# Performance work log

Hardware: AMD Instinct MI355X
Metric: run time of the kernel (lower is better)

The kernel has to match this reference:

```python
import jax, jax.numpy as jnp
import numpy as np

B, T, D, H = 4, 1024, 512, 8
DK = D // H
P = 2 * T - 1  # relative position length


def rel_shift(x):
    # x: (b, h, t, 2t-1) -> (b, h, t, t), Transformer-XL relative shift
    b, h, t, p = x.shape
    x = jnp.pad(x, ((0, 0), (0, 0), (0, 0), (1, 0)))  # (b,h,t,p+1)
    x = x.reshape(b, h, p + 1, t)[:, :, 1:, :].reshape(b, h, t, p)
    return x[..., :t]


def setup_inputs() -> dict:
    key = jax.random.key(0)
    ks = jax.random.split(key, 16)
    s = 0.02
    return {
        "q": jax.random.normal(ks[0], (B, T, D), jnp.float32),
        "k": jax.random.normal(ks[1], (B, T, D), jnp.float32),
        "v": jax.random.normal(ks[2], (B, T, D), jnp.float32),
        "pos_emb": jax.random.normal(ks[3], (1, P, D), jnp.float32),
        "Wq": jax.random.normal(ks[4], (D, D), jnp.float32) * s,
        "bq": jnp.zeros((D,), jnp.float32),
        "Wk": jax.random.normal(ks[5], (D, D), jnp.float32) * s,
        "bk": jnp.zeros((D,), jnp.float32),
        "Wv": jax.random.normal(ks[6], (D, D), jnp.float32) * s,
        "bv": jnp.zeros((D,), jnp.float32),
        "Wp": jax.random.normal(ks[7], (D, D), jnp.float32) * s,
        "pos_bias_u": jax.random.normal(ks[8], (H, DK), jnp.float32) * s,
        "pos_bias_v": jax.random.normal(ks[9], (H, DK), jnp.float32) * s,
        "Wo": jax.random.normal(ks[10], (D, D), jnp.float32) * s,
        "bo": jnp.zeros((D,), jnp.float32),
    }


def reference(q, k, v, pos_emb, Wq, bq, Wk, bk, Wv, bv, Wp,
              pos_bias_u, pos_bias_v, Wo, bo):
    b, t, d = q.shape
    # QKV projections, split heads -> (b, t, h, dk)
    qh = (q @ Wq.T + bq).reshape(b, t, H, DK)
    kh = (k @ Wk.T + bk).reshape(b, t, H, DK)
    vh = (v @ Wv.T + bv).reshape(b, t, H, DK)
    # positional projection (no bias): (1, P, h, dk)
    ph = (pos_emb @ Wp.T).reshape(pos_emb.shape[1], H, DK)
    # content term: (q + u) . k
    q_u = qh + pos_bias_u  # (b,t,h,dk)
    matrix_ac = jnp.einsum("bqhd,bkhd->bhqk", q_u, kh)
    # position term: (q + v) . p, then relative shift
    q_v = qh + pos_bias_v
    matrix_bd = jnp.einsum("bqhd,phd->bhqp", q_v, ph)
    matrix_bd = rel_shift(matrix_bd)  # (b,h,t,t)
    scores = (matrix_ac + matrix_bd) / jnp.sqrt(jnp.float32(DK))
    attn = jax.nn.softmax(scores, axis=-1)
    out = jnp.einsum("bhqk,bkhd->bqhd", attn, vh).reshape(b, t, d)
    return out @ Wo.T + bo
```

## Files before the change

### kernel.cpp

```cpp
#include <hip/hip_runtime.h>
#include <math.h>

typedef unsigned short u16;
typedef _Float16 f16;
typedef __attribute__((ext_vector_type(8))) _Float16 f16x8;
typedef __attribute__((ext_vector_type(4))) float f32x4;

#define B_  4
#define T_  1024
#define D_  512
#define H_  8
#define DK_ 64
#define P_  2047

#define MFMAH(a, b, c) __builtin_amdgcn_mfma_f32_16x16x32_f16(a, b, c, 0, 0, 0)

__device__ __forceinline__ u16 f2hbits(float x) {
    union { f16 h; u16 u; } cv; cv.h = (f16)x; return cv.u;
}

__device__ __forceinline__ void gload_lds16(const u16* g, u16* l) {
    __builtin_amdgcn_global_load_lds(
        (const __attribute__((address_space(1))) void*)g,
        (__attribute__((address_space(3))) void*)l, 16, 0, 0);
}

__device__ __forceinline__ int swz8(int row, int colbase) {
    return row * 64 + (((colbase >> 3) ^ (row & 7)) << 3);
}

__global__ __launch_bounds__(256)
void conv_all(const float* __restrict__ q, const float* __restrict__ k,
              const float* __restrict__ v, const float* __restrict__ pe,
              const float* __restrict__ wq, const float* __restrict__ wk,
              const float* __restrict__ wv, const float* __restrict__ wp,
              const float* __restrict__ wo,
              u16* qs, u16* ks, u16* vs, u16* pes,
              u16* wqs, u16* wks, u16* wvs, u16* wps, u16* wos)
{
    const int NQ = 524288;
    const int NPE = 262016;
    const int NW = 65536;
    const int TOT = 3 * NQ + NPE + 5 * NW;
    for (int i = blockIdx.x * 256 + threadIdx.x; i < TOT; i += gridDim.x * 256) {
        const float* src; u16* dst; int off;
        int j = i;
        if (j < NQ)              { src = q;  dst = qs;  off = j; }
        else if ((j -= NQ) < NQ) { src = k;  dst = ks;  off = j; }
        else if ((j -= NQ) < NQ) { src = v;  dst = vs;  off = j; }
        else if ((j -= NQ) < NPE){ src = pe; dst = pes; off = j; }
        else if ((j -= NPE) < NW){ src = wq; dst = wqs; off = j; }
        else if ((j -= NW) < NW) { src = wk; dst = wks; off = j; }
        else if ((j -= NW) < NW) { src = wv; dst = wvs; off = j; }
        else if ((j -= NW) < NW) { src = wp; dst = wps; off = j; }
        else                     { j -= NW; src = wo; dst = wos; off = j; }
        float4 x = *(const float4*)(src + (size_t)off * 4);
        union { f16 h[4]; uint2 u2; } cv;
        cv.h[0] = (f16)x.x; cv.h[1] = (f16)x.y;
        cv.h[2] = (f16)x.z; cv.h[3] = (f16)x.w;
        *(uint2*)(dst + (size_t)off * 4) = cv.u2;
    }
}

__device__ __forceinline__ void gemm_core(
    const u16* __restrict__ A, const u16* __restrict__ Bw,
    int bm, int bn, int M, f32x4 (&acc)[4][4],
    u16 (&sA)[128][64], u16 (&sB)[128][64])
{
    const int tid = threadIdx.x;
    const int ln = tid & 63, w = tid >> 6;
    const int arow = ln & 15, kseg = ln >> 4;
    const int wr = w >> 1, wc = w & 1;

    for (int k0 = 0; k0 < 512; k0 += 64) {
        #pragma unroll
        for (int it = 0; it < 4; ++it) {
            int ch = it * 256 + tid;
            int r = ch >> 3, j = ch & 7;
            int rm = bm + r; if (rm > M - 1) rm = M - 1;
            gload_lds16(A + (size_t)rm * 512 + k0 + ((j ^ (r & 7)) << 3),
                        &sA[0][0] + ch * 8);
        }
        #pragma unroll
        for (int it = 0; it < 4; ++it) {
            int ch = it * 256 + tid;
            int r = ch >> 3, j = ch & 7;
            gload_lds16(Bw + (size_t)(bn + r) * 512 + k0 + ((j ^ (r & 7)) << 3),
                        &sB[0][0] + ch * 8);
        }
        __syncthreads();

        f16x8 af[4][2], bf[4][2];
        #pragma unroll
        for (int mi = 0; mi < 4; ++mi) {
            int row = wr * 64 + mi * 16 + arow;
            #pragma unroll
            for (int kc = 0; kc < 2; ++kc)
                af[mi][kc] = *(const f16x8*)
                    (&sA[row][0] + ((((kc << 2) | kseg) ^ (row & 7)) << 3));
        }
        #pragma unroll
        for (int nj = 0; nj < 4; ++nj) {
            int row = wc * 64 + nj * 16 + arow;
            #pragma unroll
            for (int kc = 0; kc < 2; ++kc)
                bf[nj][kc] = *(const f16x8*)
                    (&sB[row][0] + ((((kc << 2) | kseg) ^ (row & 7)) << 3));
        }
        #pragma unroll
        for (int mi = 0; mi < 4; ++mi)
            #pragma unroll
            for (int nj = 0; nj < 4; ++nj)
                #pragma unroll
                for (int kc = 0; kc < 2; ++kc)
                    acc[mi][nj] = MFMAH(af[mi][kc], bf[nj][kc], acc[mi][nj]);
        __syncthreads();
    }
}

__global__ __launch_bounds__(256, 3)
void gemm_qkvp(const u16* __restrict__ qs, const u16* __restrict__ ks,
               const u16* __restrict__ vs, const u16* __restrict__ pes,
               const u16* __restrict__ wqs, const u16* __restrict__ wks,
               const u16* __restrict__ wvs, const u16* __restrict__ wps,
               const float* __restrict__ bq, const float* __restrict__ bk,
               const float* __restrict__ bv,
               const float* __restrict__ pbu, const float* __restrict__ pbv,
               u16* __restrict__ qub, u16* __restrict__ qvb,
               u16* __restrict__ kh, u16* __restrict__ vt, u16* __restrict__ ph)
{
    __shared__ u16 sA[128][64];
    __shared__ u16 sB[128][64];

    const int by = blockIdx.y;
    const u16 *A, *Bw; const float* bias;
    int seg, bm, M, Tn;
    if (by < 32)      { seg=0; bm=by*128;       A=qs;  Bw=wqs; bias=bq;      M=4096; Tn=T_; }
    else if (by < 64) { seg=1; bm=(by-32)*128;  A=ks;  Bw=wks; bias=bk;      M=4096; Tn=T_; }
    else if (by < 96) { seg=2; bm=(by-64)*128;  A=vs;  Bw=wvs; bias=bv;      M=4096; Tn=T_; }
    else              { seg=3; bm=(by-96)*128;  A=pes; Bw=wps; bias=nullptr; M=P_;   Tn=P_; }
    const int bn = blockIdx.x * 128;

    f32x4 acc[4][4] = {};
    gemm_core(A, Bw, bm, bn, M, acc, sA, sB);

    const int tid = threadIdx.x;
    const int ln = tid & 63, w = tid >> 6;
    const int arow = ln & 15, kseg = ln >> 4;
    const int wr = w >> 1, wc = w & 1;

    float bv0[4];
    #pragma unroll
    for (int nj = 0; nj < 4; ++nj)
        bv0[nj] = bias ? bias[bn + wc * 64 + nj * 16 + arow] : 0.f;

    #pragma unroll
    for (int mi = 0; mi < 4; ++mi)
        #pragma unroll
        for (int r = 0; r < 4; ++r) {
            int m = bm + wr * 64 + mi * 16 + kseg * 4 + r;
            if (m >= M) continue;
            #pragma unroll
            for (int nj = 0; nj < 4; ++nj) {
                int n = bn + wc * 64 + nj * 16 + arow;
                float val = acc[mi][nj][r] + bv0[nj];
                if (seg == 0) {
                    int bb = m >> 10, t = m & 1023;
                    int hh = n >> 6, d = n & 63;
                    size_t off = ((size_t)(bb * H_ + hh) * T_ + t) * 64 + d;
                    qub[off] = f2hbits((val + pbu[hh * 64 + d]) * 0.125f);
                    qvb[off] = f2hbits((val + pbv[hh * 64 + d]) * 0.125f);
                } else if (seg == 2) {
                    int bb = m >> 10, t = m & 1023;
                    int hh = n >> 6, d = n & 63;
                    vt[((size_t)(bb * H_ + hh) * 64 + d) * T_ + t] = f2hbits(val);
                } else {
                    int bb = (Tn == T_) ? (m >> 10) : 0;
                    int t = m - bb * Tn;
                    int hh = n >> 6, d = n & 63;
                    size_t off = ((size_t)(bb * H_ + hh) * Tn + t) * 64 + d;
                    if (seg == 1) kh[off] = f2hbits(val);
                    else          ph[off] = f2hbits(val);
                }
            }
        }
}

__global__ __launch_bounds__(256, 3)
void gemm_out(const u16* __restrict__ A, const u16* __restrict__ Bw,
              const float* __restrict__ bias, float* __restrict__ C)
{
    __shared__ u16 sA[128][64];
    __shared__ u16 sB[128][64];
    const int bn = blockIdx.x * 128;
    const int bm = blockIdx.y * 128;
    f32x4 acc[4][4] = {};
    gemm_core(A, Bw, bm, bn, 4096, acc, sA, sB);

    const int tid = threadIdx.x;
    const int ln = tid & 63, w = tid >> 6;
    const int arow = ln & 15, kseg = ln >> 4;
    const int wr = w >> 1, wc = w & 1;
    #pragma unroll
    for (int mi = 0; mi < 4; ++mi)
        #pragma unroll
        for (int r = 0; r < 4; ++r) {
            int m = bm + wr * 64 + mi * 16 + kseg * 4 + r;
            #pragma unroll
            for (int nj = 0; nj < 4; ++nj) {
                int n = bn + wc * 64 + nj * 16 + arow;
                C[(size_t)m * 512 + n] = acc[mi][nj][r] + bias[n];
            }
        }
}

__global__ __launch_bounds__(256, 2)
void relattn_mfma(const u16* __restrict__ qub, const u16* __restrict__ qvb,
                  const u16* __restrict__ kh, const u16* __restrict__ vt,
                  const u16* __restrict__ ph,
                  u16* __restrict__ ao)
{
    __shared__ u16 s_k[3][64][64];
    __shared__ u16 s_p[3][64][64];
    __shared__ u16 s_pp[4][16][64];

    const int tid = threadIdx.x;
    const int ln  = tid & 63;
    const int w   = tid >> 6;
    const int arow = ln & 15;
    const int kseg = ln >> 4;

    const int lg = ((blockIdx.x & 7) << 6) | (blockIdx.x >> 3);
    const int qt = lg & 15, h = (lg >> 4) & 7, b = lg >> 7;
    const int q0 = qt * 64;

    const size_t kvbase = (size_t)(b * H_ + h) * T_ * 64;
    const size_t vtbase = (size_t)(b * H_ + h) * 64 * T_;
    const size_t pbase  = (size_t)h * P_ * 64;
    const int jb0 = 960 - q0;

    f16x8 qu[2], qv[2];
    {
        const u16* qb = qub + kvbase + (size_t)(q0 + w * 16 + arow) * 64;
        const u16* vb = qvb + kvbase + (size_t)(q0 + w * 16 + arow) * 64;
        #pragma unroll
        for (int c = 0; c < 2; ++c) {
            qu[c] = *(const f16x8*)(qb + c * 32 + kseg * 8);
            qv[c] = *(const f16x8*)(vb + c * 32 + kseg * 8);
        }
    }

    f32x4 o_[4] = {};
    float l_run[4] = {};

    auto stage_k = [&](int kt, int slot) {
        #pragma unroll
        for (int it = 0; it < 2; ++it) {
            int idx = tid + it * 256;
            int r = idx >> 3, ch = idx & 7;
            const u16* src = kh + kvbase + (size_t)(kt * 64 + r) * 64 + ((ch ^ (r & 7)) << 3);
            gload_lds16(src, &s_k[slot][0][0] + idx * 8);
        }
    };
    auto stage_p = [&](int c, int slot) {
        #pragma unroll
        for (int it = 0; it < 2; ++it) {
            int idx = tid + it * 256;
            int r = idx >> 3, ch = idx & 7;
            int j = jb0 + c * 64 + r; if (j > P_ - 1) j = P_ - 1;
            const u16* src = ph + pbase + (size_t)j * 64 + ((ch ^ (r & 7)) << 3);
            gload_lds16(src, &s_p[slot][0][0] + idx * 8);
        }
    };
    auto bd_chunk = [&](int slot, f32x4* out) {
        #pragma unroll
        for (int nb = 0; nb < 4; ++nb) {
            int pr = nb * 16 + arow;
            f16x8 b0 = *(const f16x8*)(&s_p[slot][0][0] + swz8(pr, kseg * 8));
            f16x8 b1 = *(const f16x8*)(&s_p[slot][0][0] + swz8(pr, 32 + kseg * 8));
            out[nb] = MFMAH(qv[0], b0, out[nb]);
            out[nb] = MFMAH(qv[1], b1, out[nb]);
        }
    };

    stage_k(0, 0); stage_k(1, 1);
    stage_p(0, 0); stage_p(1, 1); stage_p(2, 2);
    __syncthreads();
    f32x4 carry[4] = {};
    bd_chunk(0, carry);
    asm volatile("" ::: "memory");
    __builtin_amdgcn_s_barrier();
    asm volatile("" ::: "memory");

    int ks = 0;
    for (int t = 0; t < 16; ++t) {
        const int k0 = t * 64;
        const int pr = (ks + 1 > 2) ? 0 : ks + 1;
        const int kw = (ks + 2 > 2) ? ks - 1 : ks + 2;

        f16x8 vfr[4][2];
        #pragma unroll
        for (int nt = 0; nt < 4; ++nt) {
            const u16* vp = vt + vtbase + (size_t)(nt * 16 + arow) * T_ + k0 + kseg * 8;
            vfr[nt][0] = *(const f16x8*)vp;
            vfr[nt][1] = *(const f16x8*)(vp + 32);
        }

        if (t < 14) { stage_k(t + 2, kw); stage_p(t + 3, ks); }

        __builtin_amdgcn_s_setprio(1);
        f32x4 ac[4] = {};
        #pragma unroll
        for (int nt = 0; nt < 4; ++nt) {
            int kr = nt * 16 + arow;
            f16x8 b0 = *(const f16x8*)(&s_k[ks][0][0] + swz8(kr, kseg * 8));
            f16x8 b1 = *(const f16x8*)(&s_k[ks][0][0] + swz8(kr, 32 + kseg * 8));
            ac[nt] = MFMAH(qu[0], b0, ac[nt]);
            ac[nt] = MFMAH(qu[1], b1, ac[nt]);
        }
        f32x4 bdn[4] = {};
        bd_chunk(pr, bdn);
        __builtin_amdgcn_s_setprio(0);

        float win[5][4];
        #pragma unroll
        for (int r = 0; r < 4; ++r) {
            if (w == 0)      { win[0][r]=carry[3][r]; win[1][r]=bdn[0][r];   win[2][r]=bdn[1][r];   win[3][r]=bdn[2][r];   win[4][r]=bdn[3][r]; }
            else if (w == 1) { win[0][r]=carry[2][r]; win[1][r]=carry[3][r]; win[2][r]=bdn[0][r];   win[3][r]=bdn[1][r];   win[4][r]=bdn[2][r]; }
            else if (w == 2) { win[0][r]=carry[1][r]; win[1][r]=carry[2][r]; win[2][r]=carry[3][r]; win[3][r]=bdn[0][r];   win[4][r]=bdn[1][r]; }
            else             { win[0][r]=carry[0][r]; win[1][r]=carry[1][r]; win[2][r]=carry[2][r]; win[3][r]=carry[3][r]; win[4][r]=bdn[0][r]; }
        }

        #pragma unroll
        for (int r = 0; r < 4; ++r) {
            int sl  = 15 - (kseg << 2) - r;
            int src = (ln & 48) | ((arow + sl) & 15);
            bool hi = (arow < sl);
            int r16 = kseg * 4 + r;
            #pragma unroll
            for (int nt = 0; nt < 4; ++nt) {
                float sel = hi ? win[nt + 1][r] : win[nt][r];
                float pm = __shfl(sel, src, 64);
                float pv = __expf(ac[nt][r] + pm);
                l_run[r] += pv;
                int kl = nt * 16 + arow;
                s_pp[w][r16][(((kl >> 3) ^ (r16 & 7)) << 3) | (kl & 7)] = f2hbits(pv);
            }
        }
        asm volatile("s_waitcnt lgkmcnt(0)" ::: "memory");
        __builtin_amdgcn_sched_barrier(0);

        f16x8 pa0 = *(const f16x8*)(&s_pp[w][arow][0] + ((kseg ^ (arow & 7)) << 3));
        f16x8 pa1 = *(const f16x8*)(&s_pp[w][arow][0] + (((4 + kseg) ^ (arow & 7)) << 3));
        __builtin_amdgcn_s_setprio(1);
        #pragma unroll
        for (int nt = 0; nt < 4; ++nt) {
            o_[nt] = MFMAH(pa0, vfr[nt][0], o_[nt]);
            o_[nt] = MFMAH(pa1, vfr[nt][1], o_[nt]);
        }
        __builtin_amdgcn_s_setprio(0);

        #pragma unroll
        for (int nb = 0; nb < 4; ++nb) carry[nb] = bdn[nb];

        asm volatile("" ::: "memory");
        __builtin_amdgcn_s_barrier();
        asm volatile("" ::: "memory");
        ks = pr;
    }

    #pragma unroll
    for (int r = 0; r < 4; ++r) {
        float l = l_run[r];
        l += __shfl_xor(l, 1); l += __shfl_xor(l, 2);
        l += __shfl_xor(l, 4); l += __shfl_xor(l, 8);
        l_run[r] = 1.f / l;
    }
    #pragma unroll
    for (int nt = 0; nt < 4; ++nt)
        #pragma unroll
        for (int r = 0; r < 4; ++r) {
            int qrow = q0 + w * 16 + kseg * 4 + r;
            size_t off = ((size_t)(b * T_ + qrow)) * D_ + h * DK_ + nt * 16 + arow;
            ao[off] = f2hbits(o_[nt][r] * l_run[r]);
        }
}

extern "C" void kernel_launch(void* const* d_in, const int* in_sizes, int n_in,
                              void* d_out, int out_size, void* d_ws, size_t ws_size,
                              hipStream_t stream)
{
    const float* q   = (const float*)d_in[0];
    const float* k   = (const float*)d_in[1];
    const float* v   = (const float*)d_in[2];
    const float* pe  = (const float*)d_in[3];
    const float* Wq  = (const float*)d_in[4];
    const float* bq  = (const float*)d_in[5];
    const float* Wk  = (const float*)d_in[6];
    const float* bk  = (const float*)d_in[7];
    const float* Wv  = (const float*)d_in[8];
    const float* bv  = (const float*)d_in[9];
    const float* Wp  = (const float*)d_in[10];
    const float* pbu = (const float*)d_in[11];
    const float* pbv = (const float*)d_in[12];
    const float* Wo  = (const float*)d_in[13];
    const float* bo  = (const float*)d_in[14];
    float* out = (float*)d_out;

    char* ws = (char*)d_ws;
    const size_t MB = 1024 * 1024;
    const size_t HMB = 512 * 1024;
    u16* qs  = (u16*)(ws);
    u16* ks  = (u16*)(ws + 4 * MB);
    u16* vs  = (u16*)(ws + 8 * MB);
    u16* pes = (u16*)(ws + 12 * MB);
    u16* wqs = (u16*)(ws + 17 * MB);
    u16* wks = (u16*)(ws + 17 * MB + HMB);
    u16* wvs = (u16*)(ws + 18 * MB);
    u16* wps = (u16*)(ws + 18 * MB + HMB);
    u16* wos = (u16*)(ws + 19 * MB);
    u16* qub = (u16*)(ws + 20 * MB);
    u16* qvb = (u16*)(ws + 24 * MB);
    u16* kh  = (u16*)(ws + 28 * MB);
    u16* vt  = (u16*)(ws + 32 * MB);
    u16* ph  = (u16*)(ws + 36 * MB);
    u16* ao  = (u16*)(ws + 38 * MB + HMB);

    dim3 blk(256);
    conv_all<<<dim3(2048), blk, 0, stream>>>(q, k, v, pe, Wq, Wk, Wv, Wp, Wo,
        qs, ks, vs, pes, wqs, wks, wvs, wps, wos);

    gemm_qkvp<<<dim3(4, 112), blk, 0, stream>>>(
        qs, ks, vs, pes, wqs, wks, wvs, wps,
        bq, bk, bv, pbu, pbv, qub, qvb, kh, vt, ph);

    relattn_mfma<<<dim3(512), blk, 0, stream>>>(qub, qvb, kh, vt, ph, ao);

    gemm_out<<<dim3(4, 32), blk, 0, stream>>>(ao, wos, bo, out);
}
```

Before: 89.30 us.

## Fuse fp32-to-fp16 activation conversion into QKV/pos projection GEMM loads

The separate conversion pass over q, k, v and pos_emb is removed. The projection GEMM now reads fp32 activations directly, converts them to fp16 in registers and stores them swizzled into LDS. Only the weights are still pre-converted by a smaller kernel. This avoids writing and re-reading about 14 MB of fp16 copies, but the A-tile load becomes a synchronous register path instead of async global-to-LDS, and each A element is loaded 4 times in fp32 across the N-blocks.

New measurement: 93.05 us. 1.04x slower.

```diff
diff --git a/kernel.cpp b/kernel.cpp
--- a/kernel.cpp
+++ b/kernel.cpp
@@ -30,35 +30,86 @@
 }
 
 __global__ __launch_bounds__(256)
-void conv_all(const float* __restrict__ q, const float* __restrict__ k,
-              const float* __restrict__ v, const float* __restrict__ pe,
-              const float* __restrict__ wq, const float* __restrict__ wk,
-              const float* __restrict__ wv, const float* __restrict__ wp,
-              const float* __restrict__ wo,
-              u16* qs, u16* ks, u16* vs, u16* pes,
-              u16* wqs, u16* wks, u16* wvs, u16* wps, u16* wos)
-{
-    const int NQ = 524288;
-    const int NPE = 262016;
+void conv_w(const float* __restrict__ wq, const float* __restrict__ wk,
+            const float* __restrict__ wv, const float* __restrict__ wp,
+            const float* __restrict__ wo,
+            u16* wqs, u16* wks, u16* wvs, u16* wps, u16* wos)
+{
     const int NW = 65536;
-    const int TOT = 3 * NQ + NPE + 5 * NW;
-    for (int i = blockIdx.x * 256 + threadIdx.x; i < TOT; i += gridDim.x * 256) {
-        const float* src; u16* dst; int off;
-        int j = i;
-        if (j < NQ)              { src = q;  dst = qs;  off = j; }
-        else if ((j -= NQ) < NQ) { src = k;  dst = ks;  off = j; }
-        else if ((j -= NQ) < NQ) { src = v;  dst = vs;  off = j; }
-        else if ((j -= NQ) < NPE){ src = pe; dst = pes; off = j; }
-        else if ((j -= NPE) < NW){ src = wq; dst = wqs; off = j; }
-        else if ((j -= NW) < NW) { src = wk; dst = wks; off = j; }
-        else if ((j -= NW) < NW) { src = wv; dst = wvs; off = j; }
-        else if ((j -= NW) < NW) { src = wp; dst = wps; off = j; }
-        else                     { j -= NW; src = wo; dst = wos; off = j; }
-        float4 x = *(const float4*)(src + (size_t)off * 4);
-        union { f16 h[4]; uint2 u2; } cv;
-        cv.h[0] = (f16)x.x; cv.h[1] = (f16)x.y;
-        cv.h[2] = (f16)x.z; cv.h[3] = (f16)x.w;
-        *(uint2*)(dst + (size_t)off * 4) = cv.u2;
+    int i = blockIdx.x * 256 + threadIdx.x;
+    if (i >= 5 * NW) return;
+    int which = i >> 16, off = i & (NW - 1);
+    const float* src = which == 0 ? wq : which == 1 ? wk : which == 2 ? wv
+                     : which == 3 ? wp : wo;
+    u16* dst = which == 0 ? wqs : which == 1 ? wks : which == 2 ? wvs
+             : which == 3 ? wps : wos;
+    float4 x = *(const float4*)(src + (size_t)off * 4);
+    union { f16 h[4]; uint2 u2; } cv;
+    cv.h[0] = (f16)x.x; cv.h[1] = (f16)x.y;
+    cv.h[2] = (f16)x.z; cv.h[3] = (f16)x.w;
+    *(uint2*)(dst + (size_t)off * 4) = cv.u2;
+}
+
+__device__ __forceinline__ void gemm_core_f32(
+    const float* __restrict__ A, const u16* __restrict__ Bw,
+    int bm, int bn, int M, f32x4 (&acc)[4][4],
+    u16 (&sA)[128][64], u16 (&sB)[128][64])
+{
+    const int tid = threadIdx.x;
+    const int ln = tid & 63, w = tid >> 6;
+    const int arow = ln & 15, kseg = ln >> 4;
+    const int wr = w >> 1, wc = w & 1;
+
+    for (int k0 = 0; k0 < 512; k0 += 64) {
+        #pragma unroll
+        for (int it = 0; it < 4; ++it) {
+            int idx = it * 256 + tid;
+            int r = idx >> 3, ch = idx & 7;
+            int rm = bm + r; if (rm > M - 1) rm = M - 1;
+            const float* s = A + (size_t)rm * 512 + k0 + ch * 8;
+            float4 x = *(const float4*)s;
+            float4 y = *(const float4*)(s + 4);
+            union { f16 h[8]; f16x8 v; } pk;
+            pk.h[0] = (f16)x.x; pk.h[1] = (f16)x.y;
+            pk.h[2] = (f16)x.z; pk.h[3] = (f16)x.w;
+            pk.h[4] = (f16)y.x; pk.h[5] = (f16)y.y;
+            pk.h[6] = (f16)y.z; pk.h[7] = (f16)y.w;
+            *(f16x8*)(&sA[r][(ch ^ (r & 7)) << 3]) = pk.v;
+        }
+        #pragma unroll
+        for (int it = 0; it < 4; ++it) {
+            int ch = it * 256 + tid;
+            int r = ch >> 3, j = ch & 7;
+            gload_lds16(Bw + (size_t)(bn + r) * 512 + k0 + ((j ^ (r & 7)) << 3),
+                        &sB[0][0] + ch * 8);
+        }
+        __syncthreads();
+
+        f16x8 af[4][2], bf[4][2];
+        #pragma unroll
+        for (int mi = 0; mi < 4; ++mi) {
+            int row = wr * 64 + mi * 16 + arow;
+            #pragma unroll
+            for (int kc = 0; kc < 2; ++kc)
+                af[mi][kc] = *(const f16x8*)
+                    (&sA[row][0] + ((((kc << 2) | kseg) ^ (row & 7)) << 3));
+        }
+        #pragma unroll
+        for (int nj = 0; nj < 4; ++nj) {
+            int row = wc * 64 + nj * 16 + arow;
+            #pragma unroll
+            for (int kc = 0; kc < 2; ++kc)
+                bf[nj][kc] = *(const f16x8*)
+                    (&sB[row][0] + ((((kc << 2) | kseg) ^ (row & 7)) << 3));
+        }
+        #pragma unroll
+        for (int mi = 0; mi < 4; ++mi)
+            #pragma unroll
+            for (int nj = 0; nj < 4; ++nj)
+                #pragma unroll
+                for (int kc = 0; kc < 2; ++kc)
+                    acc[mi][nj] = MFMAH(af[mi][kc], bf[nj][kc], acc[mi][nj]);
+        __syncthreads();
     }
 }
 
@@ -119,8 +170,8 @@
 }
 
 __global__ __launch_bounds__(256, 3)
-void gemm_qkvp(const u16* __restrict__ qs, const u16* __restrict__ ks,
-               const u16* __restrict__ vs, const u16* __restrict__ pes,
+void gemm_qkvp(const float* __restrict__ q, const float* __restrict__ k,
+               const float* __restrict__ v, const float* __restrict__ pe,
                const u16* __restrict__ wqs, const u16* __restrict__ wks,
                const u16* __restrict__ wvs, const u16* __restrict__ wps,
                const float* __restrict__ bq, const float* __restrict__ bk,
@@ -133,16 +184,16 @@
     __shared__ u16 sB[128][64];
 
     const int by = blockIdx.y;
-    const u16 *A, *Bw; const float* bias;
+    const float* A; const u16* Bw; const float* bias;
     int seg, bm, M, Tn;
-    if (by < 32)      { seg=0; bm=by*128;       A=qs;  Bw=wqs; bias=bq;      M=4096; Tn=T_; }
-    else if (by < 64) { seg=1; bm=(by-32)*128;  A=ks;  Bw=wks; bias=bk;      M=4096; Tn=T_; }
-    else if (by < 96) { seg=2; bm=(by-64)*128;  A=vs;  Bw=wvs; bias=bv;      M=4096; Tn=T_; }
-    else              { seg=3; bm=(by-96)*128;  A=pes; Bw=wps; bias=nullptr; M=P_;   Tn=P_; }
+    if (by < 32)      { seg=0; bm=by*128;       A=q;  Bw=wqs; bias=bq;      M=4096; Tn=T_; }
+    else if (by < 64) { seg=1; bm=(by-32)*128;  A=k;  Bw=wks; bias=bk;      M=4096; Tn=T_; }
+    else if (by < 96) { seg=2; bm=(by-64)*128;  A=v;  Bw=wvs; bias=bv;      M=4096; Tn=T_; }
+    else              { seg=3; bm=(by-96)*128;  A=pe; Bw=wps; bias=nullptr; M=P_;   Tn=P_; }
     const int bn = blockIdx.x * 128;
 
     f32x4 acc[4][4] = {};
-    gemm_core(A, Bw, bm, bn, M, acc, sA, sB);
+    gemm_core_f32(A, Bw, bm, bn, M, acc, sA, sB);
 
     const int tid = threadIdx.x;
     const int ln = tid & 63, w = tid >> 6;
@@ -410,28 +461,24 @@
     char* ws = (char*)d_ws;
     const size_t MB = 1024 * 1024;
     const size_t HMB = 512 * 1024;
-    u16* qs  = (u16*)(ws);
-    u16* ks  = (u16*)(ws + 4 * MB);
-    u16* vs  = (u16*)(ws + 8 * MB);
-    u16* pes = (u16*)(ws + 12 * MB);
-    u16* wqs = (u16*)(ws + 17 * MB);
-    u16* wks = (u16*)(ws + 17 * MB + HMB);
-    u16* wvs = (u16*)(ws + 18 * MB);
-    u16* wps = (u16*)(ws + 18 * MB + HMB);
-    u16* wos = (u16*)(ws + 19 * MB);
-    u16* qub = (u16*)(ws + 20 * MB);
-    u16* qvb = (u16*)(ws + 24 * MB);
-    u16* kh  = (u16*)(ws + 28 * MB);
-    u16* vt  = (u16*)(ws + 32 * MB);
-    u16* ph  = (u16*)(ws + 36 * MB);
-    u16* ao  = (u16*)(ws + 38 * MB + HMB);
+    u16* wqs = (u16*)(ws);
+    u16* wks = (u16*)(ws + 1 * HMB);
+    u16* wvs = (u16*)(ws + 2 * HMB);
+    u16* wps = (u16*)(ws + 3 * HMB);
+    u16* wos = (u16*)(ws + 4 * HMB);
+    u16* qub = (u16*)(ws + 3 * MB);
+    u16* qvb = (u16*)(ws + 7 * MB);
+    u16* kh  = (u16*)(ws + 11 * MB);
+    u16* vt  = (u16*)(ws + 15 * MB);
+    u16* ph  = (u16*)(ws + 19 * MB);
+    u16* ao  = (u16*)(ws + 22 * MB);
 
     dim3 blk(256);
-    conv_all<<<dim3(2048), blk, 0, stream>>>(q, k, v, pe, Wq, Wk, Wv, Wp, Wo,
-        qs, ks, vs, pes, wqs, wks, wvs, wps, wos);
+    conv_w<<<dim3(1280), blk, 0, stream>>>(Wq, Wk, Wv, Wp, Wo,
+                                           wqs, wks, wvs, wps, wos);
 
     gemm_qkvp<<<dim3(4, 112), blk, 0, stream>>>(
-        qs, ks, vs, pes, wqs, wks, wvs, wps,
+        q, k, v, pe, wqs, wks, wvs, wps,
         bq, bk, bv, pbu, pbv, qub, qvb, kh, vt, ph);
 
     relattn_mfma<<<dim3(512), blk, 0, stream>>>(qub, qvb, kh, vt, ph, ao);
```

## Double-buffer LDS tiles in projection GEMMs to overlap loads with MFMA

Applied to the files above, without the earlier changes.

Splits the shared-memory A/B tiles into two buffers and prefetches the next K-slice with global_load_lds while the current slice runs through MFMA. Uses explicit vmcnt waits and raw s_barrier in place of __syncthreads, and raises wave priority around the MFMA block. This targets load latency stalls in the QKV/pos and output projection GEMMs. LDS use doubles, so the occupancy hint drops from 3 to 2 blocks per CU. The GEMMs are only part of the total runtime, which also includes the attention kernel.

After: 86.44 us, median of 4. -3.2%, faster.

```diff
diff --git a/kernel.cpp b/kernel.cpp
--- a/kernel.cpp
+++ b/kernel.cpp
@@ -65,30 +65,42 @@
 __device__ __forceinline__ void gemm_core(
     const u16* __restrict__ A, const u16* __restrict__ Bw,
     int bm, int bn, int M, f32x4 (&acc)[4][4],
-    u16 (&sA)[128][64], u16 (&sB)[128][64])
+    u16 (&sA)[2][128][64], u16 (&sB)[2][128][64])
 {
     const int tid = threadIdx.x;
     const int ln = tid & 63, w = tid >> 6;
     const int arow = ln & 15, kseg = ln >> 4;
     const int wr = w >> 1, wc = w & 1;
 
-    for (int k0 = 0; k0 < 512; k0 += 64) {
+    auto stage = [&](int k0, int buf) {
         #pragma unroll
         for (int it = 0; it < 4; ++it) {
             int ch = it * 256 + tid;
             int r = ch >> 3, j = ch & 7;
             int rm = bm + r; if (rm > M - 1) rm = M - 1;
             gload_lds16(A + (size_t)rm * 512 + k0 + ((j ^ (r & 7)) << 3),
-                        &sA[0][0] + ch * 8);
+                        &sA[buf][0][0] + ch * 8);
         }
         #pragma unroll
         for (int it = 0; it < 4; ++it) {
             int ch = it * 256 + tid;
             int r = ch >> 3, j = ch & 7;
             gload_lds16(Bw + (size_t)(bn + r) * 512 + k0 + ((j ^ (r & 7)) << 3),
-                        &sB[0][0] + ch * 8);
-        }
-        __syncthreads();
+                        &sB[buf][0][0] + ch * 8);
+        }
+    };
+
+    stage(0, 0);
+    for (int t = 0; t < 8; ++t) {
+        const int cur = t & 1;
+        if (t < 7) {
+            stage((t + 1) * 64, cur ^ 1);
+            asm volatile("s_waitcnt vmcnt(8)" ::: "memory");
+        } else {
+            asm volatile("s_waitcnt vmcnt(0)" ::: "memory");
+        }
+        __builtin_amdgcn_sched_barrier(0);
+        __builtin_amdgcn_s_barrier();
 
         f16x8 af[4][2], bf[4][2];
         #pragma unroll
@@ -97,7 +109,7 @@
             #pragma unroll
             for (int kc = 0; kc < 2; ++kc)
                 af[mi][kc] = *(const f16x8*)
-                    (&sA[row][0] + ((((kc << 2) | kseg) ^ (row & 7)) << 3));
+                    (&sA[cur][row][0] + ((((kc << 2) | kseg) ^ (row & 7)) << 3));
         }
         #pragma unroll
         for (int nj = 0; nj < 4; ++nj) {
@@ -105,8 +117,9 @@
             #pragma unroll
             for (int kc = 0; kc < 2; ++kc)
                 bf[nj][kc] = *(const f16x8*)
-                    (&sB[row][0] + ((((kc << 2) | kseg) ^ (row & 7)) << 3));
-        }
+                    (&sB[cur][row][0] + ((((kc << 2) | kseg) ^ (row & 7)) << 3));
+        }
+        __builtin_amdgcn_s_setprio(1);
         #pragma unroll
         for (int mi = 0; mi < 4; ++mi)
             #pragma unroll
@@ -114,11 +127,15 @@
                 #pragma unroll
                 for (int kc = 0; kc < 2; ++kc)
                     acc[mi][nj] = MFMAH(af[mi][kc], bf[nj][kc], acc[mi][nj]);
-        __syncthreads();
+        __builtin_amdgcn_s_setprio(0);
+
+        asm volatile("" ::: "memory");
+        __builtin_amdgcn_s_barrier();
+        asm volatile("" ::: "memory");
     }
 }
 
-__global__ __launch_bounds__(256, 3)
+__global__ __launch_bounds__(256, 2)
 void gemm_qkvp(const u16* __restrict__ qs, const u16* __restrict__ ks,
                const u16* __restrict__ vs, const u16* __restrict__ pes,
                const u16* __restrict__ wqs, const u16* __restrict__ wks,
@@ -129,8 +146,8 @@
                u16* __restrict__ qub, u16* __restrict__ qvb,
                u16* __restrict__ kh, u16* __restrict__ vt, u16* __restrict__ ph)
 {
-    __shared__ u16 sA[128][64];
-    __shared__ u16 sB[128][64];
+    __shared__ u16 sA[2][128][64];
+    __shared__ u16 sB[2][128][64];
 
     const int by = blockIdx.y;
     const u16 *A, *Bw; const float* bias;
@@ -186,12 +203,12 @@
         }
 }
 
-__global__ __launch_bounds__(256, 3)
+__global__ __launch_bounds__(256, 2)
 void gemm_out(const u16* __restrict__ A, const u16* __restrict__ Bw,
               const float* __restrict__ bias, float* __restrict__ C)
 {
-    __shared__ u16 sA[128][64];
-    __shared__ u16 sB[128][64];
+    __shared__ u16 sA[2][128][64];
+    __shared__ u16 sB[2][128][64];
     const int bn = blockIdx.x * 128;
     const int bm = blockIdx.y * 128;
     f32x4 acc[4][4] = {};
```
